# Performance work log

Measured on AMD Instinct MI355X. Metric: run time of the kernel, lower is better.

## Reference

```python
import jax, jax.numpy as jnp
import numpy as np

N_PTS = 131072
IN_CH = 63
IN_CH_VIEWS = 27
WIDTH = 256
NUM_HEADS = 4
SCALE = 0.05


def setup_inputs() -> dict:
    key = jax.random.key(0)
    ks = jax.random.split(key, 12)
    H, W = NUM_HEADS, WIDTH
    inp = {
        'x': jax.random.normal(ks[0], (N_PTS, IN_CH + IN_CH_VIEWS), jnp.float32),
        'head_idx': jax.random.randint(ks[1], (N_PTS,), 0, NUM_HEADS),
        # shared trunk: layer0 63->256, layers1..3 256->256 (no skip before split_at=4)
        'W0': jax.random.normal(ks[2], (IN_CH, W), jnp.float32) * SCALE,
        'b0': jnp.zeros((W,), jnp.float32),
        'Ws': jax.random.normal(ks[3], (3, W, W), jnp.float32) * SCALE,
        'bs': jnp.zeros((3, W), jnp.float32),
        # per-head tails: g=4 in skips -> (W+63)->W, then g=5..7 W->W
        'tW0': jax.random.normal(ks[4], (H, W + IN_CH, W), jnp.float32) * SCALE,
        'tb0': jnp.zeros((H, W), jnp.float32),
        'tWs': jax.random.normal(ks[5], (H, 3, W, W), jnp.float32) * SCALE,
        'tbs': jnp.zeros((H, 3, W), jnp.float32),
        # per-head viewdirs output heads
        'featW': jax.random.normal(ks[6], (H, W, W), jnp.float32) * SCALE,
        'featb': jnp.zeros((H, W), jnp.float32),
        'alphaW': jax.random.normal(ks[7], (H, W, 1), jnp.float32) * SCALE,
        'alphab': jnp.zeros((H, 1), jnp.float32),
        'viewsW': jax.random.normal(ks[8], (H, IN_CH_VIEWS + W, W // 2), jnp.float32) * SCALE,
        'viewsb': jnp.zeros((H, W // 2), jnp.float32),
        'rgbW': jax.random.normal(ks[9], (H, W // 2, 3), jnp.float32) * SCALE,
        'rgbb': jnp.zeros((H, 3), jnp.float32),
    }
    return inp


def reference(x, head_idx, W0, b0, Ws, bs, tW0, tb0, tWs, tbs,
              featW, featb, alphaW, alphab, viewsW, viewsb, rgbW, rgbb):
    input_pts = x[:, :IN_CH]          # [N, 63]
    input_views = x[:, IN_CH:]        # [N, 27]

    # shared trunk (layers 0..3, no skip hits in this range)
    h = jax.nn.relu(input_pts @ W0 + b0)
    for i in range(Ws.shape[0]):
        h = jax.nn.relu(h @ Ws[i] + bs[i])

    # per-head tails, computed densely for ALL heads (as in the original)
    # first tail layer g=4 is a skip layer: concat input_pts
    ht = jnp.concatenate([input_pts, h], axis=-1)          # [N, 319]
    ha = jax.nn.relu(jnp.einsum('nf,hfo->nho', ht, tW0) + tb0[None])  # [N, H, 256]
    for j in range(tWs.shape[1]):
        ha = jax.nn.relu(jnp.einsum('nho,hop->nhp', ha, tWs[:, j]) + tbs[None, :, j])

    # per-head viewdir output heads
    alpha = jnp.einsum('nho,hop->nhp', ha, alphaW) + alphab[None]     # [N, H, 1]
    feat = jnp.einsum('nho,hop->nhp', ha, featW) + featb[None]        # [N, H, 256]
    views_b = jnp.broadcast_to(input_views[:, None, :], (x.shape[0], feat.shape[1], IN_CH_VIEWS))
    hv = jnp.concatenate([feat, views_b], axis=-1)                    # [N, H, 283]
    hv = jax.nn.relu(jnp.einsum('nho,hop->nhp', hv, viewsW) + viewsb[None])
    rgb = jnp.einsum('nho,hop->nhp', hv, rgbW) + rgbb[None]           # [N, H, 3]

    outs = jnp.concatenate([rgb, alpha], axis=-1)                     # [N, H, 4]
    sel = jnp.take_along_axis(outs, head_idx[:, None, None], axis=1)[:, 0]  # [N, 4]
    return sel
```

## Files before the change

kernel.cpp:

```cpp
#include <hip/hip_runtime.h>

#define N_PTS 131072
#define TILE 64
#define THREADS 512

typedef __bf16 bf16;
typedef __bf16 bf16x8 __attribute__((ext_vector_type(8)));
typedef float f32x4 __attribute__((ext_vector_type(4)));

#define WS_PERM_OFF   256
#define WS_WPACK_OFF  (256 + N_PTS * 4)
#define OFF_W0     0
#define OFF_WS     16384
#define OFF_TW0    212992
#define OFF_TWS    540672
#define OFF_FEATW  1327104
#define OFF_VIEWSW 1589248
#define TOTAL_PACK 1736704

#define PTS_BASE 0
#define H_BASE   8192
#define B_BASE   40960
#define LDS_BYTES 73728

__device__ __forceinline__ unsigned swz(unsigned base, unsigned row, unsigned rowstride,
                                        unsigned kbyte) {
  return (base + row * rowstride + kbyte) ^ ((row & 7u) << 4);
}

__device__ __forceinline__ void gload_lds16(const bf16* g, char* l) {
  __builtin_amdgcn_global_load_lds(
      (const __attribute__((address_space(1))) void*)g,
      (__attribute__((address_space(3))) void*)l, 16, 0, 0);
}

__global__ void k_pack(const float* __restrict__ W0, const float* __restrict__ Ws,
                       const float* __restrict__ tW0, const float* __restrict__ tWs,
                       const float* __restrict__ featW, const float* __restrict__ viewsW,
                       bf16* __restrict__ out, const int* __restrict__ head,
                       int* __restrict__ ctrl) {
  __shared__ int lc[4];
  if (threadIdx.x < 4) lc[threadIdx.x] = 0;
  __syncthreads();
  int gid = blockIdx.x * blockDim.x + threadIdx.x;
  if (gid < N_PTS) atomicAdd(&lc[head[gid]], 1);

  for (int idx = gid; idx < TOTAL_PACK; idx += gridDim.x * blockDim.x) {
    float v;
    if (idx < OFF_WS) {
      int o = idx >> 6, k = idx & 63;
      v = (k < 63) ? W0[k * 256 + o] : 0.f;
    } else if (idx < OFF_TW0) {
      int i = idx - OFF_WS; int l = i >> 16, r = i & 65535, o = r >> 8, k = r & 255;
      v = Ws[l * 65536 + k * 256 + o];
    } else if (idx < OFF_TWS) {
      int i = idx - OFF_TW0; int h = i / 81920, r = i % 81920, o = r / 320, k = r % 320;
      v = (k < 63) ? tW0[(h * 319 + k) * 256 + o]
                   : (k == 63 ? 0.f : tW0[(h * 319 + k - 1) * 256 + o]);
    } else if (idx < OFF_FEATW) {
      int i = idx - OFF_TWS; int hj = i >> 16, r = i & 65535, o = r >> 8, k = r & 255;
      v = tWs[(hj * 256 + k) * 256 + o];
    } else if (idx < OFF_VIEWSW) {
      int i = idx - OFF_FEATW; int h = i >> 16, r = i & 65535, o = r >> 8, k = r & 255;
      v = featW[(h * 256 + k) * 256 + o];
    } else {
      int i = idx - OFF_VIEWSW; int h = i / 36864, r = i % 36864, o = r / 288, k = r % 288;
      v = (k < 283) ? viewsW[(h * 283 + k) * 128 + o] : 0.f;
    }
    out[idx] = (bf16)v;
  }
  __syncthreads();
  if (threadIdx.x < 4 && lc[threadIdx.x]) atomicAdd(&ctrl[threadIdx.x], lc[threadIdx.x]);
}

__global__ void k_scan(int* c) {
  c[8] = 0; c[24] = 0;
  for (int h = 0; h < 4; ++h) {
    c[8 + h + 1] = c[8 + h] + c[h];
    c[16 + h] = c[8 + h];
    c[24 + h + 1] = c[24 + h] + (c[h] + TILE - 1) / TILE;
  }
}

__global__ void k_scatter(const int* __restrict__ head, int* __restrict__ c,
                          int* __restrict__ perm) {
  int p = blockIdx.x * 256 + threadIdx.x;
  int h = (p < N_PTS) ? head[p] : -1;
  int lane = threadIdx.x & 63;
  #pragma unroll
  for (int hh = 0; hh < 4; ++hh) {
    unsigned long long m = __ballot(h == hh);
    if (m == 0ull) continue;
    int leader = __builtin_ctzll(m);
    int base = 0;
    if (lane == leader) base = atomicAdd(&c[16 + hh], __popcll(m));
    base = __shfl(base, leader);
    if (h == hh) {
      int rank = __popcll(m & ((1ull << lane) - 1ull));
      perm[base + rank] = p;
    }
  }
}

template <int OUTS>
__device__ __forceinline__ void stage_B(const bf16* __restrict__ Wt, int wK, int kk,
                                        char* lds, int bufsel, int wave, int lane) {
  constexpr int ISSUES = OUTS / 128;
  #pragma unroll
  for (int s = 0; s < ISSUES; ++s) {
    int reg = wave * ISSUES + s;
    int o = reg * 16 + (lane >> 2);
    int j = lane & 3;
    const bf16* g = Wt + o * wK + kk + ((j ^ (o & 3)) << 3);
    gload_lds16(g, lds + B_BASE + bufsel * 16384 + reg * 1024);
  }
}

template <int NFRAG, bool RELU, int A0KC, int A1KC, int OUTS>
__device__ __forceinline__ void mfma_layer(char* lds, const bf16* __restrict__ Wt, int wK,
                                           const float* __restrict__ bias,
                                           int a0_base, int a0_stride,
                                           int a1_base, int a1_stride,
                                           int out_base, int out_stride,
                                           int lane, int wave) {
  const int l15 = lane & 15, l4 = lane >> 4;
  constexpr int KC = A0KC + A1KC;
  f32x4 acc[4][NFRAG];
  #pragma unroll
  for (int m = 0; m < 4; ++m)
    #pragma unroll
    for (int n = 0; n < NFRAG; ++n) acc[m][n] = (f32x4){0.f, 0.f, 0.f, 0.f};

  const int c0 = wave * (NFRAG * 16);

  stage_B<OUTS>(Wt, wK, 0, lds, 0, wave, lane);
  __syncthreads();

  #pragma unroll 1
  for (int kc = 0; kc < KC; ++kc) {
    const int buf = kc & 1;
    if (kc + 1 < KC) stage_B<OUTS>(Wt, wK, (kc + 1) * 32, lds, buf ^ 1, wave, lane);

    const int base   = (kc < A0KC) ? a0_base   : a1_base;
    const int stride = (kc < A0KC) ? a0_stride : a1_stride;
    const int kl     = ((kc < A0KC) ? kc : kc - A0KC) * 32;
    bf16x8 a[4];
    #pragma unroll
    for (int m = 0; m < 4; ++m)
      a[m] = *(const bf16x8*)(lds + swz(base, m * 16 + l15, stride, (kl + l4 * 8) * 2));

    bf16x8 b[NFRAG];
    #pragma unroll
    for (int n = 0; n < NFRAG; ++n) {
      int col = c0 + n * 16 + l15;
      b[n] = *(const bf16x8*)(lds + B_BASE + buf * 16384 + col * 64 + ((l4 ^ (col & 3)) << 4));
    }

    #pragma unroll
    for (int n = 0; n < NFRAG; ++n)
      #pragma unroll
      for (int m = 0; m < 4; ++m)
        acc[m][n] = __builtin_amdgcn_mfma_f32_16x16x32_bf16(a[m], b[n], acc[m][n], 0, 0, 0);

    __syncthreads();
  }

  #pragma unroll
  for (int n = 0; n < NFRAG; ++n) {
    int col = c0 + n * 16 + l15;
    float bv = bias[col];
    #pragma unroll
    for (int m = 0; m < 4; ++m) {
      #pragma unroll
      for (int j = 0; j < 4; ++j) {
        float v = acc[m][n][j] + bv;
        if (RELU) v = fmaxf(v, 0.f);
        int row = m * 16 + l4 * 4 + j;
        *(bf16*)(lds + swz(out_base, row, out_stride, col * 2)) = (bf16)v;
      }
    }
  }
}

__global__ __launch_bounds__(THREADS, 4) void k_main(
    const float* __restrict__ x, const int* __restrict__ ctrl, const int* __restrict__ perm,
    const bf16* __restrict__ wpack,
    const float* __restrict__ b0, const float* __restrict__ bs,
    const float* __restrict__ tb0p, const float* __restrict__ tbsp,
    const float* __restrict__ featb, const float* __restrict__ alphaW,
    const float* __restrict__ alphab, const float* __restrict__ viewsb,
    const float* __restrict__ rgbW, const float* __restrict__ rgbb,
    float* __restrict__ outp) {
  __shared__ __attribute__((aligned(16))) char lds[LDS_BYTES];
  __shared__ int pidx[TILE];
  __shared__ float alpha_s[TILE];

  const int tid = threadIdx.x;
  const int lane = tid & 63, wave = tid >> 6;

  const int tbA = ctrl[24], tbB = ctrl[25], tbC = ctrl[26], tbD = ctrl[27], tbE = ctrl[28];
  const int bid = blockIdx.x;
  if (bid >= tbE) return;
  const int hh = (bid >= tbB) + (bid >= tbC) + (bid >= tbD);
  const int tb_h = (hh == 0) ? tbA : ((hh == 1) ? tbB : ((hh == 2) ? tbC : tbD));
  const int start = ctrl[8 + hh] + (bid - tb_h) * TILE;
  const int nv = min(TILE, ctrl[8 + hh + 1] - start);

  if (tid < TILE) pidx[tid] = (tid < nv) ? perm[start + tid] : -1;
  __syncthreads();

  for (int i = tid; i < TILE * 64; i += THREADS) {
    int row = i >> 6, c = i & 63;
    int p = pidx[row];
    float v = (p >= 0 && c < 63) ? x[p * 90 + c] : 0.f;
    *(bf16*)(lds + swz(PTS_BASE, row, 128, c * 2)) = (bf16)v;
  }

  const bf16* W0p    = wpack + OFF_W0;
  const bf16* Wsp    = wpack + OFF_WS;
  const bf16* tW0p   = wpack + OFF_TW0 + hh * 81920;
  const bf16* tWsp   = wpack + OFF_TWS + hh * 3 * 65536;
  const bf16* featWp = wpack + OFF_FEATW + hh * 65536;
  const bf16* viewsWp= wpack + OFF_VIEWSW + hh * 36864;

  mfma_layer<2, true, 2, 0, 256>(lds, W0p, 64, b0, PTS_BASE, 128, 0, 0, H_BASE, 512, lane, wave);
  mfma_layer<2, true, 8, 0, 256>(lds, Wsp,          256, bs,       H_BASE, 512, 0, 0, H_BASE, 512, lane, wave);
  mfma_layer<2, true, 8, 0, 256>(lds, Wsp + 65536,  256, bs + 256, H_BASE, 512, 0, 0, H_BASE, 512, lane, wave);
  mfma_layer<2, true, 8, 0, 256>(lds, Wsp + 131072, 256, bs + 512, H_BASE, 512, 0, 0, H_BASE, 512, lane, wave);
  mfma_layer<2, true, 2, 8, 256>(lds, tW0p, 320, tb0p + hh * 256,
                                 PTS_BASE, 128, H_BASE, 512, H_BASE, 512, lane, wave);

  for (int i = tid; i < TILE * 32; i += THREADS) {
    int row = i >> 5, c = i & 31;
    int p = pidx[row];
    float v = (p >= 0 && c < 27) ? x[p * 90 + 63 + c] : 0.f;
    *(bf16*)(lds + swz(PTS_BASE, row, 128, c * 2)) = (bf16)v;
  }

  mfma_layer<2, true, 8, 0, 256>(lds, tWsp,          256, tbsp + hh * 768,       H_BASE, 512, 0, 0, H_BASE, 512, lane, wave);
  mfma_layer<2, true, 8, 0, 256>(lds, tWsp + 65536,  256, tbsp + hh * 768 + 256, H_BASE, 512, 0, 0, H_BASE, 512, lane, wave);
  mfma_layer<2, true, 8, 0, 256>(lds, tWsp + 131072, 256, tbsp + hh * 768 + 512, H_BASE, 512, 0, 0, H_BASE, 512, lane, wave);

  __syncthreads();

  if (wave < 4) {
    int p = wave * 16 + (lane & 15);
    int kq = lane >> 4;
    const float* aW = alphaW + hh * 256;
    float s = 0.f;
    for (int i = 0; i < 8; ++i) {
      int k = kq * 64 + i * 8;
      bf16x8 hv8 = *(const bf16x8*)(lds + swz(H_BASE, p, 512, k * 2));
      #pragma unroll
      for (int j = 0; j < 8; ++j) s += (float)hv8[j] * aW[k + j];
    }
    s += __shfl_xor(s, 16);
    s += __shfl_xor(s, 32);
    if (kq == 0) alpha_s[p] = s + alphab[hh];
  }

  mfma_layer<2, false, 8, 0, 256>(lds, featWp, 256, featb + hh * 256,
                                  H_BASE, 512, 0, 0, H_BASE, 512, lane, wave);
  mfma_layer<1, true, 8, 1, 128>(lds, viewsWp, 288, viewsb + hh * 128,
                                 H_BASE, 512, PTS_BASE, 128, H_BASE, 512, lane, wave);

  __syncthreads();

  if (wave < 4) {
    int p = wave * 16 + (lane & 15);
    int kq = lane >> 4;
    const float* rW = rgbW + hh * 128 * 3;
    float r0 = 0.f, r1 = 0.f, r2 = 0.f;
    for (int i = 0; i < 4; ++i) {
      int k = kq * 32 + i * 8;
      bf16x8 hv8 = *(const bf16x8*)(lds + swz(H_BASE, p, 512, k * 2));
      #pragma unroll
      for (int j = 0; j < 8; ++j) {
        float hvf = (float)hv8[j];
        r0 += hvf * rW[(k + j) * 3 + 0];
        r1 += hvf * rW[(k + j) * 3 + 1];
        r2 += hvf * rW[(k + j) * 3 + 2];
      }
    }
    r0 += __shfl_xor(r0, 16); r0 += __shfl_xor(r0, 32);
    r1 += __shfl_xor(r1, 16); r1 += __shfl_xor(r1, 32);
    r2 += __shfl_xor(r2, 16); r2 += __shfl_xor(r2, 32);
    if (kq == 0 && p < nv) {
      int pt = pidx[p];
      float4 o = make_float4(r0 + rgbb[hh * 3 + 0], r1 + rgbb[hh * 3 + 1],
                             r2 + rgbb[hh * 3 + 2], alpha_s[p]);
      *(float4*)(outp + pt * 4) = o;
    }
  }
}

extern "C" void kernel_launch(void* const* d_in, const int* in_sizes, int n_in,
                              void* d_out, int out_size, void* d_ws, size_t ws_size,
                              hipStream_t stream) {
  const float* x      = (const float*)d_in[0];
  const int*   head   = (const int*)d_in[1];
  const float* W0     = (const float*)d_in[2];
  const float* b0     = (const float*)d_in[3];
  const float* Ws     = (const float*)d_in[4];
  const float* bs     = (const float*)d_in[5];
  const float* tW0    = (const float*)d_in[6];
  const float* tb0    = (const float*)d_in[7];
  const float* tWs    = (const float*)d_in[8];
  const float* tbs    = (const float*)d_in[9];
  const float* featW  = (const float*)d_in[10];
  const float* featb  = (const float*)d_in[11];
  const float* alphaW = (const float*)d_in[12];
  const float* alphab = (const float*)d_in[13];
  const float* viewsW = (const float*)d_in[14];
  const float* viewsb = (const float*)d_in[15];
  const float* rgbW   = (const float*)d_in[16];
  const float* rgbb   = (const float*)d_in[17];

  int*  ctrl  = (int*)d_ws;
  int*  perm  = (int*)((char*)d_ws + WS_PERM_OFF);
  bf16* wpack = (bf16*)((char*)d_ws + WS_WPACK_OFF);

  hipMemsetAsync(ctrl, 0, 256, stream);
  k_pack<<<2048, 256, 0, stream>>>(W0, Ws, tW0, tWs, featW, viewsW, wpack, head, ctrl);
  k_scan<<<1, 1, 0, stream>>>(ctrl);
  k_scatter<<<N_PTS / 256, 256, 0, stream>>>(head, ctrl, perm);
  k_main<<<N_PTS / TILE + 4, THREADS, 0, stream>>>(x, ctrl, perm, wpack,
                                                   b0, bs, tb0, tbs, featb, alphaW, alphab,
                                                   viewsb, rgbW, rgbb, (float*)d_out);
}
```

Baseline: 440.6 us.

## Tile MFMA layers as 2x4 wave grid, change B swizzle, single barrier per k-step

Each layer's 8 waves now cover a 2x4 grid of output tiles (2 row fragments by 4 column fragments) instead of every wave handling all 64 rows with 2 column fragments. This cuts redundant A-fragment LDS reads and raises MFMA work per loaded operand. The loop now uses one vmcnt wait plus barrier at the top of each k-step instead of two __syncthreads, and raises wave priority around the MFMA block. The weight swizzle now XORs with (o>>1)&3 to change the LDS bank pattern, and explicit barriers are added after each layer's epilogue. The tighter synchronisation risks races if a wait is missed.

Result: faster. 423.8 us (-3.8%).

```diff
diff --git a/kernel.cpp b/kernel.cpp
--- a/kernel.cpp
+++ b/kernel.cpp
@@ -111,12 +111,12 @@
     int reg = wave * ISSUES + s;
     int o = reg * 16 + (lane >> 2);
     int j = lane & 3;
-    const bf16* g = Wt + o * wK + kk + ((j ^ (o & 3)) << 3);
+    const bf16* g = Wt + o * wK + kk + ((j ^ ((o >> 1) & 3)) << 3);
     gload_lds16(g, lds + B_BASE + bufsel * 16384 + reg * 1024);
   }
 }
 
-template <int NFRAG, bool RELU, int A0KC, int A1KC, int OUTS>
+template <int MR, int NF, bool RELU, int A0KC, int A1KC, int OUTS>
 __device__ __forceinline__ void mfma_layer(char* lds, const bf16* __restrict__ Wt, int wK,
                                            const float* __restrict__ bias,
                                            int a0_base, int a0_stride,
@@ -124,62 +124,70 @@
                                            int out_base, int out_stride,
                                            int lane, int wave) {
   const int l15 = lane & 15, l4 = lane >> 4;
+  const int wr = wave >> 2, wc = wave & 3;
   constexpr int KC = A0KC + A1KC;
-  f32x4 acc[4][NFRAG];
+  f32x4 acc[MR][NF];
   #pragma unroll
-  for (int m = 0; m < 4; ++m)
-    #pragma unroll
-    for (int n = 0; n < NFRAG; ++n) acc[m][n] = (f32x4){0.f, 0.f, 0.f, 0.f};
-
-  const int c0 = wave * (NFRAG * 16);
+  for (int m = 0; m < MR; ++m)
+    #pragma unroll
+    for (int n = 0; n < NF; ++n) acc[m][n] = (f32x4){0.f, 0.f, 0.f, 0.f};
+
+  const int r0 = wr * (MR * 16);
+  const int c0 = wc * (NF * 16);
 
   stage_B<OUTS>(Wt, wK, 0, lds, 0, wave, lane);
-  __syncthreads();
 
   #pragma unroll 1
   for (int kc = 0; kc < KC; ++kc) {
+    asm volatile("s_waitcnt vmcnt(0)" ::: "memory");
+    __builtin_amdgcn_s_barrier();
+
     const int buf = kc & 1;
     if (kc + 1 < KC) stage_B<OUTS>(Wt, wK, (kc + 1) * 32, lds, buf ^ 1, wave, lane);
 
     const int base   = (kc < A0KC) ? a0_base   : a1_base;
     const int stride = (kc < A0KC) ? a0_stride : a1_stride;
     const int kl     = ((kc < A0KC) ? kc : kc - A0KC) * 32;
-    bf16x8 a[4];
-    #pragma unroll
-    for (int m = 0; m < 4; ++m)
-      a[m] = *(const bf16x8*)(lds + swz(base, m * 16 + l15, stride, (kl + l4 * 8) * 2));
-
-    bf16x8 b[NFRAG];
-    #pragma unroll
-    for (int n = 0; n < NFRAG; ++n) {
+    bf16x8 a[MR];
+    #pragma unroll
+    for (int m = 0; m < MR; ++m)
+      a[m] = *(const bf16x8*)(lds + swz(base, r0 + m * 16 + l15, stride,
+                                        (kl + l4 * 8) * 2));
+    bf16x8 b[NF];
+    #pragma unroll
+    for (int n = 0; n < NF; ++n) {
       int col = c0 + n * 16 + l15;
-      b[n] = *(const bf16x8*)(lds + B_BASE + buf * 16384 + col * 64 + ((l4 ^ (col & 3)) << 4));
-    }
-
-    #pragma unroll
-    for (int n = 0; n < NFRAG; ++n)
+      b[n] = *(const bf16x8*)(lds + B_BASE + buf * 16384 + col * 64 +
+                              ((l4 ^ ((col >> 1) & 3)) << 4));
+    }
+
+    __builtin_amdgcn_s_setprio(1);
+    #pragma unroll
+    for (int n = 0; n < NF; ++n)
       #pragma unroll
-      for (int m = 0; m < 4; ++m)
+      for (int m = 0; m < MR; ++m)
         acc[m][n] = __builtin_amdgcn_mfma_f32_16x16x32_bf16(a[m], b[n], acc[m][n], 0, 0, 0);
-
-    __syncthreads();
-  }
+    __builtin_amdgcn_s_setprio(0);
+  }
+
+  __builtin_amdgcn_s_barrier();
 
   #pragma unroll
-  for (int n = 0; n < NFRAG; ++n) {
+  for (int n = 0; n < NF; ++n) {
     int col = c0 + n * 16 + l15;
     float bv = bias[col];
     #pragma unroll
-    for (int m = 0; m < 4; ++m) {
+    for (int m = 0; m < MR; ++m) {
       #pragma unroll
       for (int j = 0; j < 4; ++j) {
         float v = acc[m][n][j] + bv;
         if (RELU) v = fmaxf(v, 0.f);
-        int row = m * 16 + l4 * 4 + j;
+        int row = r0 + m * 16 + l4 * 4 + j;
         *(bf16*)(lds + swz(out_base, row, out_stride, col * 2)) = (bf16)v;
       }
     }
   }
+  __syncthreads();
 }
 
 __global__ __launch_bounds__(THREADS, 4) void k_main(
@@ -215,6 +223,7 @@
     float v = (p >= 0 && c < 63) ? x[p * 90 + c] : 0.f;
     *(bf16*)(lds + swz(PTS_BASE, row, 128, c * 2)) = (bf16)v;
   }
+  __syncthreads();
 
   const bf16* W0p    = wpack + OFF_W0;
   const bf16* Wsp    = wpack + OFF_WS;
@@ -223,12 +232,12 @@
   const bf16* featWp = wpack + OFF_FEATW + hh * 65536;
   const bf16* viewsWp= wpack + OFF_VIEWSW + hh * 36864;
 
-  mfma_layer<2, true, 2, 0, 256>(lds, W0p, 64, b0, PTS_BASE, 128, 0, 0, H_BASE, 512, lane, wave);
-  mfma_layer<2, true, 8, 0, 256>(lds, Wsp,          256, bs,       H_BASE, 512, 0, 0, H_BASE, 512, lane, wave);
-  mfma_layer<2, true, 8, 0, 256>(lds, Wsp + 65536,  256, bs + 256, H_BASE, 512, 0, 0, H_BASE, 512, lane, wave);
-  mfma_layer<2, true, 8, 0, 256>(lds, Wsp + 131072, 256, bs + 512, H_BASE, 512, 0, 0, H_BASE, 512, lane, wave);
-  mfma_layer<2, true, 2, 8, 256>(lds, tW0p, 320, tb0p + hh * 256,
-                                 PTS_BASE, 128, H_BASE, 512, H_BASE, 512, lane, wave);
+  mfma_layer<2, 4, true, 2, 0, 256>(lds, W0p, 64, b0, PTS_BASE, 128, 0, 0, H_BASE, 512, lane, wave);
+  mfma_layer<2, 4, true, 8, 0, 256>(lds, Wsp,          256, bs,       H_BASE, 512, 0, 0, H_BASE, 512, lane, wave);
+  mfma_layer<2, 4, true, 8, 0, 256>(lds, Wsp + 65536,  256, bs + 256, H_BASE, 512, 0, 0, H_BASE, 512, lane, wave);
+  mfma_layer<2, 4, true, 8, 0, 256>(lds, Wsp + 131072, 256, bs + 512, H_BASE, 512, 0, 0, H_BASE, 512, lane, wave);
+  mfma_layer<2, 4, true, 2, 8, 256>(lds, tW0p, 320, tb0p + hh * 256,
+                                    PTS_BASE, 128, H_BASE, 512, H_BASE, 512, lane, wave);
 
   for (int i = tid; i < TILE * 32; i += THREADS) {
     int row = i >> 5, c = i & 31;
@@ -236,12 +245,11 @@
     float v = (p >= 0 && c < 27) ? x[p * 90 + 63 + c] : 0.f;
     *(bf16*)(lds + swz(PTS_BASE, row, 128, c * 2)) = (bf16)v;
   }
-
-  mfma_layer<2, true, 8, 0, 256>(lds, tWsp,          256, tbsp + hh * 768,       H_BASE, 512, 0, 0, H_BASE, 512, lane, wave);
-  mfma_layer<2, true, 8, 0, 256>(lds, tWsp + 65536,  256, tbsp + hh * 768 + 256, H_BASE, 512, 0, 0, H_BASE, 512, lane, wave);
-  mfma_layer<2, true, 8, 0, 256>(lds, tWsp + 131072, 256, tbsp + hh * 768 + 512, H_BASE, 512, 0, 0, H_BASE, 512, lane, wave);
-
-  __syncthreads();
+  __syncthreads();
+
+  mfma_layer<2, 4, true, 8, 0, 256>(lds, tWsp,          256, tbsp + hh * 768,       H_BASE, 512, 0, 0, H_BASE, 512, lane, wave);
+  mfma_layer<2, 4, true, 8, 0, 256>(lds, tWsp + 65536,  256, tbsp + hh * 768 + 256, H_BASE, 512, 0, 0, H_BASE, 512, lane, wave);
+  mfma_layer<2, 4, true, 8, 0, 256>(lds, tWsp + 131072, 256, tbsp + hh * 768 + 512, H_BASE, 512, 0, 0, H_BASE, 512, lane, wave);
 
   if (wave < 4) {
     int p = wave * 16 + (lane & 15);
@@ -259,12 +267,10 @@
     if (kq == 0) alpha_s[p] = s + alphab[hh];
   }
 
-  mfma_layer<2, false, 8, 0, 256>(lds, featWp, 256, featb + hh * 256,
-                                  H_BASE, 512, 0, 0, H_BASE, 512, lane, wave);
-  mfma_layer<1, true, 8, 1, 128>(lds, viewsWp, 288, viewsb + hh * 128,
-                                 H_BASE, 512, PTS_BASE, 128, H_BASE, 512, lane, wave);
-
-  __syncthreads();
+  mfma_layer<2, 4, false, 8, 0, 256>(lds, featWp, 256, featb + hh * 256,
+                                     H_BASE, 512, 0, 0, H_BASE, 512, lane, wave);
+  mfma_layer<2, 2, true, 8, 1, 128>(lds, viewsWp, 288, viewsb + hh * 128,
+                                    H_BASE, 512, PTS_BASE, 128, H_BASE, 512, lane, wave);
 
   if (wave < 4) {
     int p = wave * 16 + (lane & 15);
```
